# Optimization experiments

Hardware: AMD Instinct MI355X
Metric: run time of the kernel (lower is better)

Reference implementation:

```python
import jax, jax.numpy as jnp
import numpy as np

BATCH = 4096
DIM = 256
TEMPERATURE = 0.5
EPS = 1e-8  # torch CosineSimilarity norm clamp


def setup_inputs() -> dict:
    key = jax.random.key(0)
    k1, k2 = jax.random.split(key)
    zA = jax.random.normal(k1, (BATCH, DIM), dtype=jnp.float32)
    zB = jax.random.normal(k2, (BATCH, DIM), dtype=jnp.float32)
    return {"zA": zA, "zB": zB}


def reference(zA, zB):
    b = zA.shape[0]
    N = 2 * b
    z = jnp.concatenate([zA, zB], axis=0)                      # [N, D]
    norm = jnp.maximum(jnp.linalg.norm(z, axis=1, keepdims=True), EPS)
    zn = z / norm
    # cosine-similarity matrix via normalize + GEMM (same math as the
    # broadcasted CosineSimilarity(dim=2) in the original)
    sim = (zn @ zn.T) / TEMPERATURE                            # [N, N]

    idx = jnp.arange(N)
    pos = sim[idx, (idx + b) % N]                              # diag(+b) ++ diag(-b)

    # CE with label 0 over logits=[pos, negatives]; the logit set per row is
    # exactly {all j != i} (pos partner included once), so mask only the diagonal.
    neg_inf = jnp.finfo(sim.dtype).min
    masked = jnp.where(jnp.eye(N, dtype=bool), neg_inf, sim)
    per_row = jax.nn.logsumexp(masked, axis=1) - pos           # [N]
    loss = jnp.sum(per_row) / N                                # reduction='sum' / N
    return loss
```

## Files before the change

### kernel.cpp

```cpp
#include <hip/hip_runtime.h>
#include <hip/hip_bf16.h>

#define N_ROWS 8192
#define BATCH 4096
#define DIM 256

#define MTILE 256
#define CCHUNK 512
#define NCHUNK 16
#define CT 16
#define LDSROW 528
#define LDSBUF (CT * LDSROW)
#define KEXP 2.8853900817779268f

typedef __attribute__((ext_vector_type(8))) short bfrag8;
typedef __attribute__((ext_vector_type(4))) float facc4;

__global__ __launch_bounds__(256) void normalize_kernel(
    const float* __restrict__ zA, const float* __restrict__ zB,
    __hip_bfloat16* __restrict__ zn) {
    int tid = threadIdx.x;
    int wave = tid >> 6, lane = tid & 63;
    int row = blockIdx.x * 4 + wave;
    const float* src = (row < BATCH) ? (zA + (size_t)row * DIM)
                                     : (zB + (size_t)(row - BATCH) * DIM);
    float4 v = ((const float4*)src)[lane];
    float ss = v.x * v.x + v.y * v.y + v.z * v.z + v.w * v.w;
    #pragma unroll
    for (int m = 32; m; m >>= 1) ss += __shfl_xor(ss, m);
    float inv = 1.0f / fmaxf(sqrtf(ss), 1e-8f);
    union { ushort4 u; __hip_bfloat16 h[4]; } o;
    o.h[0] = __float2bfloat16(v.x * inv);
    o.h[1] = __float2bfloat16(v.y * inv);
    o.h[2] = __float2bfloat16(v.z * inv);
    o.h[3] = __float2bfloat16(v.w * inv);
    ((ushort4*)zn)[(size_t)row * (DIM / 4) + lane] = o.u;
}

__global__ __launch_bounds__(256, 2) void ntxent_main(
    const __hip_bfloat16* __restrict__ zn_,
    float* __restrict__ ep, float* __restrict__ pp) {
    const char* zn = (const char*)zn_;
    __shared__ char lds[2 * LDSBUF] __attribute__((aligned(16)));
    int tid = threadIdx.x, lane = tid & 63, wave = tid >> 6;
    int quad = lane >> 4, l15 = lane & 15;
    int row0 = blockIdx.x * MTILE + wave * 64;
    int chunk = blockIdx.y;
    int cc = chunk * CCHUNK;

    bfrag8 a[4][8];
    #pragma unroll
    for (int s = 0; s < 4; s++) {
        const char* ap = zn + (size_t)(row0 + s * 16 + l15) * 512 + quad * 16;
        #pragma unroll
        for (int ks = 0; ks < 8; ks++)
            a[s][ks] = *(const bfrag8*)(ap + ks * 64);
    }

    float es[4][4], ps[4][4];
    #pragma unroll
    for (int s = 0; s < 4; s++)
        #pragma unroll
        for (int r = 0; r < 4; r++) { es[s][r] = 0.f; ps[s][r] = 0.f; }

    int col0 = tid >> 5, j0 = tid & 31;
    unsigned lofs0 = col0 * LDSROW + j0 * 16;
    unsigned lofs1 = (col0 + 8) * LDSROW + j0 * 16;
    unsigned gofs0 = col0 * 512 + j0 * 16;
    unsigned gofs1 = (col0 + 8) * 512 + j0 * 16;
    const char* gbase = zn + (size_t)cc * 512;

    {
        uint4 r0 = *(const uint4*)(gbase + gofs0);
        uint4 r1 = *(const uint4*)(gbase + gofs1);
        *(uint4*)(lds + lofs0) = r0;
        *(uint4*)(lds + lofs1) = r1;
    }
    __syncthreads();

    const int NT = CCHUNK / CT;
    for (int t = 0; t < NT; t++) {
        char* cur = lds + (t & 1) * LDSBUF;
        char* nxt = lds + ((t + 1) & 1) * LDSBUF;
        uint4 s0, s1;
        if (t + 1 < NT) {
            const char* g = gbase + (size_t)(t + 1) * CT * 512;
            s0 = *(const uint4*)(g + gofs0);
            s1 = *(const uint4*)(g + gofs1);
        }
        const char* bp = cur + l15 * LDSROW + quad * 16;
        bfrag8 bf[8];
        #pragma unroll
        for (int ks = 0; ks < 8; ks++)
            bf[ks] = *(const bfrag8*)(bp + ks * 64);

        facc4 acc[4];
        #pragma unroll
        for (int s = 0; s < 4; s++) acc[s] = (facc4){0.f, 0.f, 0.f, 0.f};
        #pragma unroll
        for (int ks = 0; ks < 8; ks++)
            #pragma unroll
            for (int s = 0; s < 4; s++)
                acc[s] = __builtin_amdgcn_mfma_f32_16x16x32_bf16(a[s][ks], bf[ks], acc[s], 0, 0, 0);

        int ctile = cc + t * CT;
        int gcol = ctile + l15;
        bool isdiag = (ctile >> 6) == (row0 >> 6);
        bool ispos  = (ctile >> 6) == ((row0 ^ BATCH) >> 6);
        if (isdiag) {
            #pragma unroll
            for (int s = 0; s < 4; s++)
                #pragma unroll
                for (int r = 0; r < 4; r++) {
                    int grow = row0 + s * 16 + quad * 4 + r;
                    float e = __builtin_amdgcn_exp2f(acc[s][r] * KEXP);
                    if (gcol == grow) e = 0.0f;
                    es[s][r] += e;
                }
        } else if (ispos) {
            #pragma unroll
            for (int s = 0; s < 4; s++)
                #pragma unroll
                for (int r = 0; r < 4; r++) {
                    int grow = row0 + s * 16 + quad * 4 + r;
                    float d = acc[s][r];
                    es[s][r] += __builtin_amdgcn_exp2f(d * KEXP);
                    if (gcol == (grow ^ BATCH)) ps[s][r] += d;
                }
        } else {
            #pragma unroll
            for (int s = 0; s < 4; s++)
                #pragma unroll
                for (int r = 0; r < 4; r++)
                    es[s][r] += __builtin_amdgcn_exp2f(acc[s][r] * KEXP);
        }

        if (t + 1 < NT) {
            *(uint4*)(nxt + lofs0) = s0;
            *(uint4*)(nxt + lofs1) = s1;
        }
        __syncthreads();
    }

    bool poswave = (((row0 ^ BATCH) >> 9) == chunk);
    #pragma unroll
    for (int s = 0; s < 4; s++)
        #pragma unroll
        for (int r = 0; r < 4; r++) {
            float e = es[s][r], p = ps[s][r];
            #pragma unroll
            for (int m = 1; m < 16; m <<= 1) {
                e += __shfl_xor(e, m);
                p += __shfl_xor(p, m);
            }
            if (l15 == 0) {
                int grow = row0 + s * 16 + quad * 4 + r;
                ep[(size_t)chunk * N_ROWS + grow] = e;
                if (poswave) pp[grow] = p;
            }
        }
}

__global__ __launch_bounds__(256) void finalize_kernel(
    const float* __restrict__ ep, const float* __restrict__ pp,
    float* __restrict__ out) {
    int tid = threadIdx.x;
    int i = blockIdx.x * 256 + tid;
    float e = 0.0f;
    #pragma unroll
    for (int c = 0; c < NCHUNK; c++) e += ep[(size_t)c * N_ROWS + i];
    float v = __logf(e) - 2.0f * pp[i];
    #pragma unroll
    for (int m = 32; m; m >>= 1) v += __shfl_xor(v, m);
    __shared__ float wsum[4];
    if ((tid & 63) == 0) wsum[tid >> 6] = v;
    __syncthreads();
    if (tid == 0)
        atomicAdd(out, (wsum[0] + wsum[1] + wsum[2] + wsum[3]) * (1.0f / N_ROWS));
}

extern "C" void kernel_launch(void* const* d_in, const int* in_sizes, int n_in,
                              void* d_out, int out_size, void* d_ws, size_t ws_size,
                              hipStream_t stream) {
    const float* zA = (const float*)d_in[0];
    const float* zB = (const float*)d_in[1];
    float* out = (float*)d_out;
    char* ws = (char*)d_ws;
    __hip_bfloat16* zn = (__hip_bfloat16*)ws;
    float* ep = (float*)(ws + (size_t)N_ROWS * DIM * 2);
    float* pp = ep + (size_t)NCHUNK * N_ROWS;

    hipMemsetAsync(out, 0, sizeof(float), stream);
    normalize_kernel<<<N_ROWS / 4, 256, 0, stream>>>(zA, zB, zn);
    dim3 grid(N_ROWS / MTILE, NCHUNK);
    ntxent_main<<<grid, 256, 0, stream>>>(zn, ep, pp);
    finalize_kernel<<<N_ROWS / 256, 256, 0, stream>>>(ep, pp, out);
}
```

Measured before the change: 103.5 us.

## Exploit similarity-matrix symmetry by computing only upper-triangular block tiles

The kernel now launches one block per upper-triangular 128x128 tile pair (bi<=bj) and uses symmetry of zn·znᵀ, so each off-diagonal tile's exp values feed both row sums and column sums (column sums via LDS colbuf). This roughly halves the MFMA and exp work. Tiles are smaller (128 rows, 4 blocks/SM target), the positive-pair logit is written directly for both partners, and finalize sums 64 partial slices instead of 16. In exchange it adds per-tile cross-lane column reductions, more partial-sum traffic, and a triangular index decode with float sqrt.

After: 127.7 us. 1.23x slower.

```diff
diff --git a/kernel.cpp b/kernel.cpp
--- a/kernel.cpp
+++ b/kernel.cpp
@@ -5,10 +5,10 @@
 #define BATCH 4096
 #define DIM 256
 
-#define MTILE 256
-#define CCHUNK 512
-#define NCHUNK 16
+#define NB 64
+#define BR 128
 #define CT 16
+#define NT 8
 #define LDSROW 528
 #define LDSBUF (CT * LDSROW)
 #define KEXP 2.8853900817779268f
@@ -37,38 +37,47 @@
     ((ushort4*)zn)[(size_t)row * (DIM / 4) + lane] = o.u;
 }
 
-__global__ __launch_bounds__(256, 2) void ntxent_main(
+__global__ __launch_bounds__(256, 4) void ntxent_main(
     const __hip_bfloat16* __restrict__ zn_,
     float* __restrict__ ep, float* __restrict__ pp) {
     const char* zn = (const char*)zn_;
     __shared__ char lds[2 * LDSBUF] __attribute__((aligned(16)));
+    __shared__ float colbuf[4][BR];
     int tid = threadIdx.x, lane = tid & 63, wave = tid >> 6;
     int quad = lane >> 4, l15 = lane & 15;
-    int row0 = blockIdx.x * MTILE + wave * 64;
-    int chunk = blockIdx.y;
-    int cc = chunk * CCHUNK;
-
-    bfrag8 a[4][8];
-    #pragma unroll
-    for (int s = 0; s < 4; s++) {
+
+    int k = blockIdx.x;
+    int bi = (int)(0.5f * (129.0f - sqrtf(16641.0f - 8.0f * (float)k)));
+    if (bi < 0) bi = 0;
+    if (bi > NB - 1) bi = NB - 1;
+    while (bi * (129 - bi) / 2 > k) --bi;
+    while ((bi + 1) * (128 - bi) / 2 <= k) ++bi;
+    int bj = bi + (k - bi * (129 - bi) / 2);
+    bool diagblk = (bi == bj);
+
+    int row0 = bi * BR + wave * 32;
+
+    bfrag8 a[2][8];
+    #pragma unroll
+    for (int s = 0; s < 2; s++) {
         const char* ap = zn + (size_t)(row0 + s * 16 + l15) * 512 + quad * 16;
         #pragma unroll
         for (int ks = 0; ks < 8; ks++)
             a[s][ks] = *(const bfrag8*)(ap + ks * 64);
     }
 
-    float es[4][4], ps[4][4];
-    #pragma unroll
-    for (int s = 0; s < 4; s++)
-        #pragma unroll
-        for (int r = 0; r < 4; r++) { es[s][r] = 0.f; ps[s][r] = 0.f; }
+    float es[2][4];
+    #pragma unroll
+    for (int s = 0; s < 2; s++)
+        #pragma unroll
+        for (int r = 0; r < 4; r++) es[s][r] = 0.f;
 
     int col0 = tid >> 5, j0 = tid & 31;
     unsigned lofs0 = col0 * LDSROW + j0 * 16;
     unsigned lofs1 = (col0 + 8) * LDSROW + j0 * 16;
     unsigned gofs0 = col0 * 512 + j0 * 16;
     unsigned gofs1 = (col0 + 8) * 512 + j0 * 16;
-    const char* gbase = zn + (size_t)cc * 512;
+    const char* gbase = zn + (size_t)bj * BR * 512;
 
     {
         uint4 r0 = *(const uint4*)(gbase + gofs0);
@@ -78,7 +87,6 @@
     }
     __syncthreads();
 
-    const int NT = CCHUNK / CT;
     for (int t = 0; t < NT; t++) {
         char* cur = lds + (t & 1) * LDSBUF;
         char* nxt = lds + ((t + 1) & 1) * LDSBUF;
@@ -89,50 +97,71 @@
             s1 = *(const uint4*)(g + gofs1);
         }
         const char* bp = cur + l15 * LDSROW + quad * 16;
-        bfrag8 bf[8];
-        #pragma unroll
-        for (int ks = 0; ks < 8; ks++)
+
+        facc4 acc[2];
+        acc[0] = (facc4){0.f, 0.f, 0.f, 0.f};
+        acc[1] = (facc4){0.f, 0.f, 0.f, 0.f};
+        bfrag8 bf[4];
+        #pragma unroll
+        for (int ks = 0; ks < 4; ks++)
             bf[ks] = *(const bfrag8*)(bp + ks * 64);
-
-        facc4 acc[4];
-        #pragma unroll
-        for (int s = 0; s < 4; s++) acc[s] = (facc4){0.f, 0.f, 0.f, 0.f};
-        #pragma unroll
-        for (int ks = 0; ks < 8; ks++)
-            #pragma unroll
-            for (int s = 0; s < 4; s++)
-                acc[s] = __builtin_amdgcn_mfma_f32_16x16x32_bf16(a[s][ks], bf[ks], acc[s], 0, 0, 0);
-
-        int ctile = cc + t * CT;
+        #pragma unroll
+        for (int ks = 0; ks < 4; ks++) {
+            acc[0] = __builtin_amdgcn_mfma_f32_16x16x32_bf16(a[0][ks], bf[ks], acc[0], 0, 0, 0);
+            acc[1] = __builtin_amdgcn_mfma_f32_16x16x32_bf16(a[1][ks], bf[ks], acc[1], 0, 0, 0);
+        }
+        #pragma unroll
+        for (int ks = 0; ks < 4; ks++)
+            bf[ks] = *(const bfrag8*)(bp + 256 + ks * 64);
+        #pragma unroll
+        for (int ks = 0; ks < 4; ks++) {
+            acc[0] = __builtin_amdgcn_mfma_f32_16x16x32_bf16(a[0][ks + 4], bf[ks], acc[0], 0, 0, 0);
+            acc[1] = __builtin_amdgcn_mfma_f32_16x16x32_bf16(a[1][ks + 4], bf[ks], acc[1], 0, 0, 0);
+        }
+
+        int ctile = bj * BR + t * CT;
         int gcol = ctile + l15;
-        bool isdiag = (ctile >> 6) == (row0 >> 6);
-        bool ispos  = (ctile >> 6) == ((row0 ^ BATCH) >> 6);
+        float ce = 0.0f;
+        bool isdiag = (ctile >> 5) == (row0 >> 5);
+        bool ispos  = (ctile >> 5) == ((row0 ^ BATCH) >> 5);
+
         if (isdiag) {
             #pragma unroll
-            for (int s = 0; s < 4; s++)
+            for (int s = 0; s < 2; s++)
                 #pragma unroll
                 for (int r = 0; r < 4; r++) {
                     int grow = row0 + s * 16 + quad * 4 + r;
                     float e = __builtin_amdgcn_exp2f(acc[s][r] * KEXP);
                     if (gcol == grow) e = 0.0f;
-                    es[s][r] += e;
-                }
-        } else if (ispos) {
-            #pragma unroll
-            for (int s = 0; s < 4; s++)
-                #pragma unroll
-                for (int r = 0; r < 4; r++) {
-                    int grow = row0 + s * 16 + quad * 4 + r;
-                    float d = acc[s][r];
-                    es[s][r] += __builtin_amdgcn_exp2f(d * KEXP);
-                    if (gcol == (grow ^ BATCH)) ps[s][r] += d;
+                    es[s][r] += e; ce += e;
                 }
         } else {
             #pragma unroll
-            for (int s = 0; s < 4; s++)
+            for (int s = 0; s < 2; s++)
                 #pragma unroll
-                for (int r = 0; r < 4; r++)
-                    es[s][r] += __builtin_amdgcn_exp2f(acc[s][r] * KEXP);
+                for (int r = 0; r < 4; r++) {
+                    float e = __builtin_amdgcn_exp2f(acc[s][r] * KEXP);
+                    es[s][r] += e; ce += e;
+                }
+            if (ispos) {
+                #pragma unroll
+                for (int s = 0; s < 2; s++)
+                    #pragma unroll
+                    for (int r = 0; r < 4; r++) {
+                        int grow = row0 + s * 16 + quad * 4 + r;
+                        if (gcol == (grow ^ BATCH)) {
+                            float d = acc[s][r];
+                            pp[grow] = d;
+                            pp[grow ^ BATCH] = d;
+                        }
+                    }
+            }
+        }
+
+        if (!diagblk) {
+            ce += __shfl_xor(ce, 16);
+            ce += __shfl_xor(ce, 32);
+            if (lane < 16) colbuf[wave][t * CT + l15] = ce;
         }
 
         if (t + 1 < NT) {
@@ -142,23 +171,21 @@
         __syncthreads();
     }
 
-    bool poswave = (((row0 ^ BATCH) >> 9) == chunk);
-    #pragma unroll
-    for (int s = 0; s < 4; s++)
+    #pragma unroll
+    for (int s = 0; s < 2; s++)
         #pragma unroll
         for (int r = 0; r < 4; r++) {
-            float e = es[s][r], p = ps[s][r];
+            float e = es[s][r];
             #pragma unroll
-            for (int m = 1; m < 16; m <<= 1) {
-                e += __shfl_xor(e, m);
-                p += __shfl_xor(p, m);
-            }
-            if (l15 == 0) {
-                int grow = row0 + s * 16 + quad * 4 + r;
-                ep[(size_t)chunk * N_ROWS + grow] = e;
-                if (poswave) pp[grow] = p;
-            }
-        }
+            for (int m = 1; m < 16; m <<= 1) e += __shfl_xor(e, m);
+            if (l15 == 0)
+                ep[(size_t)bj * N_ROWS + row0 + s * 16 + quad * 4 + r] = e;
+        }
+
+    if (!diagblk && tid < BR) {
+        float v = colbuf[0][tid] + colbuf[1][tid] + colbuf[2][tid] + colbuf[3][tid];
+        ep[(size_t)bi * N_ROWS + bj * BR + tid] = v;
+    }
 }
 
 __global__ __launch_bounds__(256) void finalize_kernel(
@@ -168,7 +195,7 @@
     int i = blockIdx.x * 256 + tid;
     float e = 0.0f;
     #pragma unroll
-    for (int c = 0; c < NCHUNK; c++) e += ep[(size_t)c * N_ROWS + i];
+    for (int s = 0; s < NB; s++) e += ep[(size_t)s * N_ROWS + i];
     float v = __logf(e) - 2.0f * pp[i];
     #pragma unroll
     for (int m = 32; m; m >>= 1) v += __shfl_xor(v, m);
@@ -188,11 +215,10 @@
     char* ws = (char*)d_ws;
     __hip_bfloat16* zn = (__hip_bfloat16*)ws;
     float* ep = (float*)(ws + (size_t)N_ROWS * DIM * 2);
-    float* pp = ep + (size_t)NCHUNK * N_ROWS;
+    float* pp = ep + (size_t)NB * N_ROWS;
 
     hipMemsetAsync(out, 0, sizeof(float), stream);
     normalize_kernel<<<N_ROWS / 4, 256, 0, stream>>>(zA, zB, zn);
-    dim3 grid(N_ROWS / MTILE, NCHUNK);
-    ntxent_main<<<grid, 256, 0, stream>>>(zn, ep, pp);
+    ntxent_main<<<NB * (NB + 1) / 2, 256, 0, stream>>>(zn, ep, pp);
     finalize_kernel<<<N_ROWS / 256, 256, 0, stream>>>(ep, pp, out);
 }
```
